# Kernel optimization log

Hardware: AMD Instinct MI355X
Metric: run time of the kernel (lower is better)

## Reference

```python
import jax, jax.numpy as jnp
import numpy as np

B, C, D, H, W = 4, 128, 16, 16, 16
HID = 128
EPS = 1e-5


def setup_inputs() -> dict:
    key = jax.random.key(0)
    ks = jax.random.split(key, 10)
    s = 1.0 / np.sqrt(C)
    return {
        "x": jax.random.normal(ks[0], (B, C, D, H, W), dtype=jnp.float32),
        "Wq": jax.random.normal(ks[1], (HID, C), dtype=jnp.float32) * s,
        "bq": jax.random.normal(ks[2], (HID,), dtype=jnp.float32) * s,
        "Wk": jax.random.normal(ks[3], (HID, C), dtype=jnp.float32) * s,
        "bk": jax.random.normal(ks[4], (HID,), dtype=jnp.float32) * s,
        "Wv": jax.random.normal(ks[5], (HID, C), dtype=jnp.float32) * s,
        "bv": jax.random.normal(ks[6], (HID,), dtype=jnp.float32) * s,
        "bn_weight": jax.random.normal(ks[7], (HID,), dtype=jnp.float32),
        "bn_bias": jax.random.normal(ks[8], (HID,), dtype=jnp.float32),
        "gamma": jax.random.normal(ks[9], (1,), dtype=jnp.float32),
    }


def reference(x, Wq, bq, Wk, bk, Wv, bv, bn_weight, bn_bias, gamma):
    b, c, d, h, w = x.shape
    n = d * h * w
    xf = x.reshape(b, c, n)  # [B, C, N]
    # 1x1 conv3d == per-voxel linear: [B, hid, N]
    q = jnp.einsum("hc,bcn->bnh", Wq, xf) + bq  # [B, N, hid] (query permuted)
    k = jnp.einsum("hc,bcn->bhn", Wk, xf) + bk[None, :, None]  # [B, hid, N]
    v = jnp.einsum("hc,bcn->bhn", Wv, xf) + bv[None, :, None]  # [B, hid, N]
    # unscaled attention scores [B, N, N], softmax over last dim
    attn = jax.nn.softmax(jnp.einsum("bih,bhj->bij", q, k), axis=-1)
    # out[b,h,i] = sum_j v[b,h,j] * attn[b,i,j]
    out = jnp.einsum("bhj,bij->bhi", v, attn)  # [B, hid, N]
    # BatchNorm3d (training mode): per-channel stats over (B, N), biased var
    mean = jnp.mean(out, axis=(0, 2), keepdims=True)
    var = jnp.mean(jnp.square(out - mean), axis=(0, 2), keepdims=True)
    out = (out - mean) * jax.lax.rsqrt(var + EPS)
    out = out * bn_weight[None, :, None] + bn_bias[None, :, None]
    out = gamma[0] * out.reshape(b, c, d, h, w) + x
    return out
```

## Files before the change

kernel.cpp:

```cpp
#include <hip/hip_runtime.h>


#define NV 4096
#define LOG2E 1.44269504088896340736f
#define EPSV 1e-5f

typedef float f32x4 __attribute__((ext_vector_type(4)));
typedef short bf16x8 __attribute__((ext_vector_type(8)));
typedef unsigned short u16x4 __attribute__((ext_vector_type(4)));
typedef unsigned short u16x8 __attribute__((ext_vector_type(8)));
typedef unsigned int u32x2 __attribute__((ext_vector_type(2)));

static __device__ __forceinline__ unsigned short f2bf(float f) {
    union { float f; unsigned u; } v; v.f = f;
    unsigned r = v.u + 0x7FFFu + ((v.u >> 16) & 1u);
    return (unsigned short)(r >> 16);
}
static __device__ __forceinline__ float bf2f(unsigned short u) {
    union { unsigned u; float f; } v; v.u = ((unsigned)u) << 16; return v.f;
}
static __device__ __forceinline__ unsigned fbits(float f) {
    union { float f; unsigned u; } v; v.f = f; return v.u;
}

__global__ __launch_bounds__(256) void projx_kernel(
    const float* __restrict__ x,
    const float* __restrict__ Wq, const float* __restrict__ Wk,
    const float* __restrict__ Wv,
    const float* __restrict__ bq, const float* __restrict__ bk,
    const float* __restrict__ bv,
    unsigned short* __restrict__ Qb, unsigned short* __restrict__ Kb,
    unsigned short* __restrict__ Vb)
{
    __shared__ unsigned short xt[64 * 136];
    __shared__ unsigned short Wl[128 * 136];
    const int bid = blockIdx.x;
    const int m = bid >> 8, b = (bid >> 6) & 3, n0 = (bid & 63) << 6;
    const int t = threadIdx.x, w = t >> 6, lane = t & 63;
    const int quad = lane >> 4, l16 = lane & 15;

    const float* Wm = (m == 0) ? Wq : ((m == 1) ? Wk : Wv);
    const float* bias = (m == 0) ? bq : ((m == 1) ? bk : bv);

    #pragma unroll
    for (int it = 0; it < 8; ++it) {
        const int e = (it << 8) + t;
        const int c = e >> 4, i4 = (e & 15) << 2;
        const float4 xv = *(const float4*)(x + (((b << 7) + c) << 12) + n0 + i4);
        xt[(i4 + 0) * 136 + c] = f2bf(xv.x);
        xt[(i4 + 1) * 136 + c] = f2bf(xv.y);
        xt[(i4 + 2) * 136 + c] = f2bf(xv.z);
        xt[(i4 + 3) * 136 + c] = f2bf(xv.w);
    }
    #pragma unroll
    for (int it = 0; it < 16; ++it) {
        const int idx = it * 1024 + (t << 2);
        const float4 wv4 = *(const float4*)(Wm + idx);
        const int h = idx >> 7, c = idx & 127;
        u16x4 pk;
        pk[0] = f2bf(wv4.x); pk[1] = f2bf(wv4.y);
        pk[2] = f2bf(wv4.z); pk[3] = f2bf(wv4.w);
        *(u16x4*)(Wl + h * 136 + c) = pk;
    }
    __syncthreads();

    bf16x8 af[4];
    {
        const int il = (w << 4) + l16;
        #pragma unroll
        for (int ck = 0; ck < 4; ++ck)
            af[ck] = *(const bf16x8*)(xt + il * 136 + (ck << 5) + (quad << 3));
    }
    if (m == 2) __syncthreads();

    #pragma unroll
    for (int s = 0; s < 8; ++s) {
        const int h = (s << 4) + l16;
        f32x4 acc = {0.f, 0.f, 0.f, 0.f};
        #pragma unroll
        for (int ck = 0; ck < 4; ++ck) {
            const bf16x8 wf = *(const bf16x8*)(Wl + h * 136 + (ck << 5) + (quad << 3));
            acc = __builtin_amdgcn_mfma_f32_16x16x32_bf16(af[ck], wf, acc, 0, 0, 0);
        }
        const float bval = bias[h];
        if (m == 2) {
            #pragma unroll
            for (int r = 0; r < 4; ++r)
                xt[h * 66 + (w << 4) + (quad << 2) + r] = f2bf(acc[r] + bval);
        } else {
            #pragma unroll
            for (int r = 0; r < 4; ++r) {
                float val = acc[r] + bval;
                if (m == 0) val *= LOG2E;
                xt[((w << 4) + (quad << 2) + r) * 136 + h] = f2bf(val);
            }
        }
    }
    __syncthreads();
    if (m == 2) {
        #pragma unroll
        for (int it = 0; it < 32; ++it) {
            const int e = it * 256 + t;
            const int h = e >> 6, il = e & 63;
            Vb[(((b << 7) + h) << 12) + n0 + il] = xt[h * 66 + il];
        }
    } else {
        unsigned short* dst = (m == 0) ? Qb : Kb;
        #pragma unroll
        for (int it = 0; it < 4; ++it) {
            const int e = (it << 8) + t;
            const int row = e >> 4, c8 = (e & 15) << 3;
            *(bf16x8*)(dst + (((b << 12) + n0 + row) << 7) + c8) =
                *(const bf16x8*)(xt + row * 136 + c8);
        }
    }
}

template<int NSL>
__global__ __launch_bounds__(256, 2) void flash_kernel(
    const unsigned short* __restrict__ Qb,
    const unsigned short* __restrict__ Kb,
    const unsigned short* __restrict__ Vb,
    unsigned short* __restrict__ Opart, float* __restrict__ lpart,
    unsigned short* __restrict__ Obuf)
{
    __shared__ unsigned short Kt[64 * 128];
    __shared__ unsigned short Vt[128 * 64];
    __shared__ unsigned short pA[4][32 * 72];
    constexpr int NB = (NSL == 6) ? 768 : NSL * 128;
    const int bid = ((blockIdx.x & 7) * (NB >> 3)) + (blockIdx.x >> 3);
    const int sl = bid >> 7, b = (bid >> 5) & 3, ic = bid & 31;
    const int t = threadIdx.x, w = t >> 6, lane = t & 63;
    const int quad = lane >> 4, l16 = lane & 15;
    const int iw = (ic << 7) + (w << 5);

    int T, joff;
    if constexpr (NSL == 6) {
        T = 11 - (sl >= 4);
        joff = sl * 11 - ((sl >= 5) ? 1 : 0);
    } else {
        T = (NV / NSL) >> 6;
        joff = sl * T;
    }
    const int jbase = joff << 6;
    unsigned short* pAw = pA[w];

    const int ktg = t & 15, ktj = t >> 4;
    const int vtg = t & 7,  vth = t >> 3;
    const int kswz = (ktg ^ ktj) << 3;
    const int vswz = (vtg ^ (vth & 7)) << 3;

    bf16x8 qf[2][4];
    #pragma unroll
    for (int half = 0; half < 2; ++half) {
        const unsigned short* qp =
            Qb + (((b << 12) + iw + (half << 4) + l16) << 7) + (quad << 3);
        #pragma unroll
        for (int ck = 0; ck < 4; ++ck) qf[half][ck] = *(const bf16x8*)(qp + (ck << 5));
    }
    f32x4 Oacc[2][8];
    #pragma unroll
    for (int half = 0; half < 2; ++half)
        #pragma unroll
        for (int s = 0; s < 8; ++s) Oacc[half][s] = (f32x4){0.f, 0.f, 0.f, 0.f};
    float lsum0 = 0.f, lsum1 = 0.f;

    const unsigned short* Kbb = Kb + ((long)b << 19);
    const unsigned short* Vbb = Vb + ((long)b << 19);
    const int T8 = T;

    bf16x8 sk[4], sv[4];
    #pragma unroll
    for (int r = 0; r < 4; ++r)
        sk[r] = *(const bf16x8*)(Kbb + ((jbase + (r << 4) + ktj) << 7) + (ktg << 3));
    #pragma unroll
    for (int r = 0; r < 4; ++r)
        sv[r] = *(const bf16x8*)(Vbb + (((r << 5) + vth) << 12) + jbase + (vtg << 3));

    for (int t8 = 0; t8 < T8; ++t8) {
        const int j0 = jbase + (t8 << 6);

        __syncthreads();
        #pragma unroll
        for (int r = 0; r < 4; ++r)
            *(bf16x8*)(Kt + (((r << 4) + ktj) << 7) + kswz) = sk[r];
        #pragma unroll
        for (int r = 0; r < 4; ++r)
            *(bf16x8*)(Vt + (((r << 5) + vth) << 6) + vswz) = sv[r];
        __syncthreads();

        if (t8 + 1 < T8) {
            const int j1 = j0 + 64;
            #pragma unroll
            for (int r = 0; r < 4; ++r)
                sk[r] = *(const bf16x8*)(Kbb + ((j1 + (r << 4) + ktj) << 7) + (ktg << 3));
            #pragma unroll
            for (int r = 0; r < 4; ++r)
                sv[r] = *(const bf16x8*)(Vbb + (((r << 5) + vth) << 12) + j1 + (vtg << 3));
        }

        #pragma unroll
        for (int js = 0; js < 4; ++js) {
            bf16x8 kf[4];
            const int krow = ((js << 4) + l16) << 7;
            #pragma unroll
            for (int ck = 0; ck < 4; ++ck)
                kf[ck] = *(const bf16x8*)(Kt + krow + ((((ck << 2) + quad) ^ l16) << 3));
            f32x4 a0 = {0.f, 0.f, 0.f, 0.f}, a1 = {0.f, 0.f, 0.f, 0.f};
            #pragma unroll
            for (int ck = 0; ck < 4; ++ck) {
                a0 = __builtin_amdgcn_mfma_f32_16x16x32_bf16(kf[ck], qf[0][ck], a0, 0, 0, 0);
                a1 = __builtin_amdgcn_mfma_f32_16x16x32_bf16(kf[ck], qf[1][ck], a1, 0, 0, 0);
            }
            f32x4 e0, e1;
            #pragma unroll
            for (int r = 0; r < 4; ++r) {
                e0[r] = __builtin_amdgcn_exp2f(a0[r]);
                e1[r] = __builtin_amdgcn_exp2f(a1[r]);
            }
            lsum0 += (e0[0] + e0[1]) + (e0[2] + e0[3]);
            lsum1 += (e1[0] + e1[1]) + (e1[2] + e1[3]);
            u32x2 pk0, pk1;
            pk0[0] = __builtin_amdgcn_perm(fbits(e0[1]), fbits(e0[0]), 0x07060302u);
            pk0[1] = __builtin_amdgcn_perm(fbits(e0[3]), fbits(e0[2]), 0x07060302u);
            pk1[0] = __builtin_amdgcn_perm(fbits(e1[1]), fbits(e1[0]), 0x07060302u);
            pk1[1] = __builtin_amdgcn_perm(fbits(e1[3]), fbits(e1[2]), 0x07060302u);
            const int jc = (js << 4) + (quad << 2);
            *(u32x2*)(pAw + l16 * 72 + jc)        = pk0;
            *(u32x2*)(pAw + (16 + l16) * 72 + jc) = pk1;
        }
        bf16x8 pf[2][2];
        #pragma unroll
        for (int half = 0; half < 2; ++half)
            #pragma unroll
            for (int kh = 0; kh < 2; ++kh)
                pf[half][kh] = *(const bf16x8*)(pAw + ((half << 4) + l16) * 72 +
                                                (kh << 5) + (quad << 3));
        #pragma unroll
        for (int s = 0; s < 8; ++s) {
            const int vrow = ((s << 4) + l16) << 6;
            const bf16x8 v0 = *(const bf16x8*)(Vt + vrow + ((quad ^ (l16 & 7)) << 3));
            const bf16x8 v1 = *(const bf16x8*)(Vt + vrow + (((4 + quad) ^ (l16 & 7)) << 3));
            Oacc[0][s] = __builtin_amdgcn_mfma_f32_16x16x32_bf16(v0, pf[0][0], Oacc[0][s], 0, 0, 0);
            Oacc[0][s] = __builtin_amdgcn_mfma_f32_16x16x32_bf16(v1, pf[0][1], Oacc[0][s], 0, 0, 0);
            Oacc[1][s] = __builtin_amdgcn_mfma_f32_16x16x32_bf16(v0, pf[1][0], Oacc[1][s], 0, 0, 0);
            Oacc[1][s] = __builtin_amdgcn_mfma_f32_16x16x32_bf16(v1, pf[1][1], Oacc[1][s], 0, 0, 0);
        }
    }

    float l0 = lsum0; l0 += __shfl_xor(l0, 16); l0 += __shfl_xor(l0, 32);
    float l1 = lsum1; l1 += __shfl_xor(l1, 16); l1 += __shfl_xor(l1, 32);

    if (NSL == 1) {
        const float rl0 = 1.f / l0, rl1 = 1.f / l1;
        #pragma unroll
        for (int s = 0; s < 8; ++s)
            #pragma unroll
            for (int r = 0; r < 4; ++r) {
                const int h = (s << 4) + (quad << 2) + r;
                Obuf[(((b << 7) + h) << 12) + iw + l16]      = f2bf(Oacc[0][s][r] * rl0);
                Obuf[(((b << 7) + h) << 12) + iw + 16 + l16] = f2bf(Oacc[1][s][r] * rl1);
            }
    } else {
        const int slb = (sl << 2) + b;
        if (quad == 0) {
            lpart[(slb << 12) + iw + l16]      = l0;
            lpart[(slb << 12) + iw + 16 + l16] = l1;
        }
        unsigned short* Ob = Opart + ((long)slb << 19);
        #pragma unroll
        for (int half = 0; half < 2; ++half)
            #pragma unroll
            for (int s = 0; s < 8; ++s)
                #pragma unroll
                for (int r = 0; r < 4; ++r) {
                    const int h = (s << 4) + (quad << 2) + r;
                    Ob[(h << 12) + iw + (half << 4) + l16] = f2bf(Oacc[half][s][r]);
                }
    }
}

template<int NSL>
__global__ __launch_bounds__(1024) void mf_kernel(
    const unsigned short* __restrict__ Opart, const float* __restrict__ lpart,
    const float* __restrict__ x, const float* __restrict__ bnw,
    const float* __restrict__ bnb, const float* __restrict__ gammap,
    float* __restrict__ out)
{
    const int h = blockIdx.x;
    const int t = threadIdx.x;
    const int b = t >> 8;
    const int i0 = (t & 255) << 4;

    float A[16], L[16];
    #pragma unroll
    for (int k = 0; k < 16; ++k) { A[k] = 0.f; L[k] = 0.f; }
    #pragma unroll
    for (int sl = 0; sl < NSL; ++sl) {
        const int slb = (sl << 2) + b;
        const u16x8 u0 = *(const u16x8*)(Opart + ((long)slb << 19) + ((long)h << 12) + i0);
        const u16x8 u1 = *(const u16x8*)(Opart + ((long)slb << 19) + ((long)h << 12) + i0 + 8);
        const float* lp = lpart + (slb << 12) + i0;
        #pragma unroll
        for (int k = 0; k < 8; ++k) { A[k] += bf2f(u0[k]); A[8 + k] += bf2f(u1[k]); }
        #pragma unroll
        for (int k = 0; k < 4; ++k) {
            const float4 lv = *(const float4*)(lp + (k << 2));
            L[(k << 2) + 0] += lv.x; L[(k << 2) + 1] += lv.y;
            L[(k << 2) + 2] += lv.z; L[(k << 2) + 3] += lv.w;
        }
    }
    float o[16], s = 0.f, ss = 0.f;
    #pragma unroll
    for (int k = 0; k < 16; ++k) {
        o[k] = A[k] / L[k];
        s += o[k]; ss += o[k] * o[k];
    }
    #pragma unroll
    for (int off = 32; off; off >>= 1) {
        s  += __shfl_down(s, off);
        ss += __shfl_down(ss, off);
    }
    __shared__ float rs[16], rss[16], fin[2];
    const int wid = t >> 6;
    if ((t & 63) == 0) { rs[wid] = s; rss[wid] = ss; }
    __syncthreads();
    if (t == 0) {
        float s2 = 0.f, ss2 = 0.f;
        #pragma unroll
        for (int k = 0; k < 16; ++k) { s2 += rs[k]; ss2 += rss[k]; }
        fin[0] = s2; fin[1] = ss2;
    }
    __syncthreads();
    const float inv = 1.f / 16384.f;
    const float mean = fin[0] * inv;
    const float var  = fin[1] * inv - mean * mean;
    const float g = gammap[0];
    const float scale = bnw[h] * rsqrtf(var + EPSV);
    const float a  = g * scale;
    const float bb = g * (bnb[h] - mean * scale);

    const float* xp = x + (((b << 7) + h) << 12) + i0;
    float* op = out + (((b << 7) + h) << 12) + i0;
    #pragma unroll
    for (int k = 0; k < 4; ++k) {
        const float4 xv = *(const float4*)(xp + (k << 2));
        float4 r;
        r.x = o[(k << 2) + 0] * a + bb + xv.x;
        r.y = o[(k << 2) + 1] * a + bb + xv.y;
        r.z = o[(k << 2) + 2] * a + bb + xv.z;
        r.w = o[(k << 2) + 3] * a + bb + xv.w;
        *(float4*)(op + (k << 2)) = r;
    }
}

__global__ __launch_bounds__(1024) void mf1_kernel(
    const unsigned short* __restrict__ Obuf,
    const float* __restrict__ x, const float* __restrict__ bnw,
    const float* __restrict__ bnb, const float* __restrict__ gammap,
    float* __restrict__ out)
{
    const int h = blockIdx.x;
    const int t = threadIdx.x;
    const int b = t >> 8;
    const int i0 = (t & 255) << 4;
    const u16x8 u0 = *(const u16x8*)(Obuf + (((b << 7) + h) << 12) + i0);
    const u16x8 u1 = *(const u16x8*)(Obuf + (((b << 7) + h) << 12) + i0 + 8);
    float o[16], s = 0.f, ss = 0.f;
    #pragma unroll
    for (int k = 0; k < 8; ++k) { o[k] = bf2f(u0[k]); o[8 + k] = bf2f(u1[k]); }
    #pragma unroll
    for (int k = 0; k < 16; ++k) { s += o[k]; ss += o[k] * o[k]; }
    #pragma unroll
    for (int off = 32; off; off >>= 1) {
        s  += __shfl_down(s, off);
        ss += __shfl_down(ss, off);
    }
    __shared__ float rs[16], rss[16], fin[2];
    const int wid = t >> 6;
    if ((t & 63) == 0) { rs[wid] = s; rss[wid] = ss; }
    __syncthreads();
    if (t == 0) {
        float s2 = 0.f, ss2 = 0.f;
        #pragma unroll
        for (int k = 0; k < 16; ++k) { s2 += rs[k]; ss2 += rss[k]; }
        fin[0] = s2; fin[1] = ss2;
    }
    __syncthreads();
    const float inv = 1.f / 16384.f;
    const float mean = fin[0] * inv;
    const float var  = fin[1] * inv - mean * mean;
    const float g = gammap[0];
    const float scale = bnw[h] * rsqrtf(var + EPSV);
    const float a  = g * scale;
    const float bb = g * (bnb[h] - mean * scale);
    const float* xp = x + (((b << 7) + h) << 12) + i0;
    float* op = out + (((b << 7) + h) << 12) + i0;
    #pragma unroll
    for (int k = 0; k < 4; ++k) {
        const float4 xv = *(const float4*)(xp + (k << 2));
        float4 r;
        r.x = o[(k << 2) + 0] * a + bb + xv.x;
        r.y = o[(k << 2) + 1] * a + bb + xv.y;
        r.z = o[(k << 2) + 2] * a + bb + xv.z;
        r.w = o[(k << 2) + 3] * a + bb + xv.w;
        *(float4*)(op + (k << 2)) = r;
    }
}

extern "C" void kernel_launch(void* const* d_in, const int* in_sizes, int n_in,
                              void* d_out, int out_size, void* d_ws, size_t ws_size,
                              hipStream_t stream) {
    const float* x   = (const float*)d_in[0];
    const float* Wq  = (const float*)d_in[1];
    const float* bq  = (const float*)d_in[2];
    const float* Wk  = (const float*)d_in[3];
    const float* bk  = (const float*)d_in[4];
    const float* Wv  = (const float*)d_in[5];
    const float* bv  = (const float*)d_in[6];
    const float* bnw = (const float*)d_in[7];
    const float* bnb = (const float*)d_in[8];
    const float* gam = (const float*)d_in[9];
    float* out = (float*)d_out;

    char* ws = (char*)d_ws;
    unsigned short* Obuf = (unsigned short*)(ws);
    unsigned short* Qb   = (unsigned short*)(ws + (4u  << 20));
    unsigned short* Kb   = (unsigned short*)(ws + (8u  << 20));
    unsigned short* Vb   = (unsigned short*)(ws + (12u << 20));
    float*          lpart = (float*)(ws + (16u << 20) + (128u << 10));
    unsigned short* Opart = (unsigned short*)(ws + (17u << 20));

    int nsl = 1;
    if      (ws_size >= (17ull << 20) + (32ull << 20)) nsl = 6;
    else if (ws_size >= (17ull << 20) + (16ull << 20)) nsl = 4;
    else if (ws_size >= (17ull << 20) + (8ull  << 20)) nsl = 2;

    projx_kernel<<<768, 256, 0, stream>>>(x, Wq, Wk, Wv, bq, bk, bv, Qb, Kb, Vb);
    if (nsl == 6) {
        flash_kernel<6><<<768, 256, 0, stream>>>(Qb, Kb, Vb, Opart, lpart, Obuf);
        mf_kernel<6><<<128, 1024, 0, stream>>>(Opart, lpart, x, bnw, bnb, gam, out);
    } else if (nsl == 4) {
        flash_kernel<4><<<512, 256, 0, stream>>>(Qb, Kb, Vb, Opart, lpart, Obuf);
        mf_kernel<4><<<128, 1024, 0, stream>>>(Opart, lpart, x, bnw, bnb, gam, out);
    } else if (nsl == 2) {
        flash_kernel<2><<<256, 256, 0, stream>>>(Qb, Kb, Vb, Opart, lpart, Obuf);
        mf_kernel<2><<<128, 1024, 0, stream>>>(Opart, lpart, x, bnw, bnb, gam, out);
    } else {
        flash_kernel<1><<<128, 256, 0, stream>>>(Qb, Kb, Vb, Opart, lpart, Obuf);
        mf1_kernel<<<128, 1024, 0, stream>>>(Obuf, x, bnw, bnb, gam, out);
    }
}
```

Measured before the change: 148.7 us.

## Use 32x32x16 MFMA with permlane32 swap to keep P in registers

Rewrites the flash attention inner loop around 32x32x16 bf16 MFMA tiles. The exponentiated scores are repacked in registers with v_permlane32_swap, so P is fed to the PV matmul without the per-wave LDS staging buffer. It also adds s_setprio around the MFMA sections and drops the 6-way split, so the default path becomes the 4-way split with 512 blocks. This cuts LDS traffic and instruction count per tile, at the cost of higher register pressure from 64 accumulator floats plus the 16-wide score tile, and a different load balance without the 6-split.

```diff
diff --git a/kernel.cpp b/kernel.cpp
--- a/kernel.cpp
+++ b/kernel.cpp
@@ -6,10 +6,10 @@
 #define EPSV 1e-5f
 
 typedef float f32x4 __attribute__((ext_vector_type(4)));
+typedef float f32x16 __attribute__((ext_vector_type(16)));
 typedef short bf16x8 __attribute__((ext_vector_type(8)));
 typedef unsigned short u16x4 __attribute__((ext_vector_type(4)));
 typedef unsigned short u16x8 __attribute__((ext_vector_type(8)));
-typedef unsigned int u32x2 __attribute__((ext_vector_type(2)));
 
 static __device__ __forceinline__ unsigned short f2bf(float f) {
     union { float f; unsigned u; } v; v.f = f;
@@ -126,48 +126,36 @@
 {
     __shared__ unsigned short Kt[64 * 128];
     __shared__ unsigned short Vt[128 * 64];
-    __shared__ unsigned short pA[4][32 * 72];
-    constexpr int NB = (NSL == 6) ? 768 : NSL * 128;
+    constexpr int NB = NSL * 128;
     const int bid = ((blockIdx.x & 7) * (NB >> 3)) + (blockIdx.x >> 3);
     const int sl = bid >> 7, b = (bid >> 5) & 3, ic = bid & 31;
     const int t = threadIdx.x, w = t >> 6, lane = t & 63;
-    const int quad = lane >> 4, l16 = lane & 15;
+    const int l32 = lane & 31, hi = lane >> 5;
     const int iw = (ic << 7) + (w << 5);
 
-    int T, joff;
-    if constexpr (NSL == 6) {
-        T = 11 - (sl >= 4);
-        joff = sl * 11 - ((sl >= 5) ? 1 : 0);
-    } else {
-        T = (NV / NSL) >> 6;
-        joff = sl * T;
-    }
-    const int jbase = joff << 6;
-    unsigned short* pAw = pA[w];
+    const int T = (NV / NSL) >> 6;
+    const int jbase = sl * T << 6;
 
     const int ktg = t & 15, ktj = t >> 4;
     const int vtg = t & 7,  vth = t >> 3;
     const int kswz = (ktg ^ ktj) << 3;
     const int vswz = (vtg ^ (vth & 7)) << 3;
 
-    bf16x8 qf[2][4];
-    #pragma unroll
-    for (int half = 0; half < 2; ++half) {
-        const unsigned short* qp =
-            Qb + (((b << 12) + iw + (half << 4) + l16) << 7) + (quad << 3);
-        #pragma unroll
-        for (int ck = 0; ck < 4; ++ck) qf[half][ck] = *(const bf16x8*)(qp + (ck << 5));
-    }
-    f32x4 Oacc[2][8];
-    #pragma unroll
-    for (int half = 0; half < 2; ++half)
-        #pragma unroll
-        for (int s = 0; s < 8; ++s) Oacc[half][s] = (f32x4){0.f, 0.f, 0.f, 0.f};
-    float lsum0 = 0.f, lsum1 = 0.f;
+    bf16x8 qf[8];
+    {
+        const unsigned short* qp = Qb + (((b << 12) + iw + l32) << 7) + (hi << 3);
+        #pragma unroll
+        for (int kc = 0; kc < 8; ++kc) qf[kc] = *(const bf16x8*)(qp + (kc << 4));
+    }
+    f32x16 Oacc[4];
+    #pragma unroll
+    for (int ht = 0; ht < 4; ++ht)
+        #pragma unroll
+        for (int r = 0; r < 16; ++r) Oacc[ht][r] = 0.f;
+    float lsum = 0.f;
 
     const unsigned short* Kbb = Kb + ((long)b << 19);
     const unsigned short* Vbb = Vb + ((long)b << 19);
-    const int T8 = T;
 
     bf16x8 sk[4], sv[4];
     #pragma unroll
@@ -177,7 +165,7 @@
     for (int r = 0; r < 4; ++r)
         sv[r] = *(const bf16x8*)(Vbb + (((r << 5) + vth) << 12) + jbase + (vtg << 3));
 
-    for (int t8 = 0; t8 < T8; ++t8) {
+    for (int t8 = 0; t8 < T; ++t8) {
         const int j0 = jbase + (t8 << 6);
 
         __syncthreads();
@@ -189,7 +177,7 @@
             *(bf16x8*)(Vt + (((r << 5) + vth) << 6) + vswz) = sv[r];
         __syncthreads();
 
-        if (t8 + 1 < T8) {
+        if (t8 + 1 < T) {
             const int j1 = j0 + 64;
             #pragma unroll
             for (int r = 0; r < 4; ++r)
@@ -200,83 +188,77 @@
         }
 
         #pragma unroll
-        for (int js = 0; js < 4; ++js) {
-            bf16x8 kf[4];
-            const int krow = ((js << 4) + l16) << 7;
-            #pragma unroll
-            for (int ck = 0; ck < 4; ++ck)
-                kf[ck] = *(const bf16x8*)(Kt + krow + ((((ck << 2) + quad) ^ l16) << 3));
-            f32x4 a0 = {0.f, 0.f, 0.f, 0.f}, a1 = {0.f, 0.f, 0.f, 0.f};
-            #pragma unroll
-            for (int ck = 0; ck < 4; ++ck) {
-                a0 = __builtin_amdgcn_mfma_f32_16x16x32_bf16(kf[ck], qf[0][ck], a0, 0, 0, 0);
-                a1 = __builtin_amdgcn_mfma_f32_16x16x32_bf16(kf[ck], qf[1][ck], a1, 0, 0, 0);
+        for (int jt = 0; jt < 2; ++jt) {
+            const unsigned short* kr = Kt + (((jt << 5) + l32) << 7);
+            f32x16 a;
+            #pragma unroll
+            for (int r = 0; r < 16; ++r) a[r] = 0.f;
+            __builtin_amdgcn_s_setprio(1);
+            #pragma unroll
+            for (int kc = 0; kc < 8; ++kc) {
+                const bf16x8 kf = *(const bf16x8*)(kr + ((((kc << 1) + hi) ^ (l32 & 15)) << 3));
+                a = __builtin_amdgcn_mfma_f32_32x32x16_bf16(kf, qf[kc], a, 0, 0, 0);
             }
-            f32x4 e0, e1;
-            #pragma unroll
-            for (int r = 0; r < 4; ++r) {
-                e0[r] = __builtin_amdgcn_exp2f(a0[r]);
-                e1[r] = __builtin_amdgcn_exp2f(a1[r]);
+            __builtin_amdgcn_s_setprio(0);
+            float e[16];
+            #pragma unroll
+            for (int r = 0; r < 16; ++r) e[r] = __builtin_amdgcn_exp2f(a[r]);
+            lsum += ((e[0] + e[1]) + (e[2] + e[3])) + ((e[4] + e[5]) + (e[6] + e[7]))
+                  + ((e[8] + e[9]) + (e[10] + e[11])) + ((e[12] + e[13]) + (e[14] + e[15]));
+            unsigned wd[8];
+            #pragma unroll
+            for (int g = 0; g < 8; ++g)
+                wd[g] = __builtin_amdgcn_perm(fbits(e[2 * g + 1]), fbits(e[2 * g]),
+                                              0x07060302u);
+            unsigned a0 = wd[0], a2 = wd[2];
+            asm("v_permlane32_swap_b32 %0, %1" : "+v"(a0), "+v"(a2));
+            unsigned a1 = wd[1], a3 = wd[3];
+            asm("v_permlane32_swap_b32 %0, %1" : "+v"(a1), "+v"(a3));
+            unsigned b0 = wd[4], b2 = wd[6];
+            asm("v_permlane32_swap_b32 %0, %1" : "+v"(b0), "+v"(b2));
+            unsigned b1 = wd[5], b3 = wd[7];
+            asm("v_permlane32_swap_b32 %0, %1" : "+v"(b1), "+v"(b3));
+            union PW { unsigned w[4]; bf16x8 v; };
+            PW p0, p1;
+            p0.w[0] = a0; p0.w[1] = a1; p0.w[2] = a2; p0.w[3] = a3;
+            p1.w[0] = b0; p1.w[1] = b1; p1.w[2] = b2; p1.w[3] = b3;
+            const bf16x8 pa0 = p0.v, pa1 = p1.v;
+            __builtin_amdgcn_s_setprio(1);
+            #pragma unroll
+            for (int ht = 0; ht < 4; ++ht) {
+                const unsigned short* vr = Vt + (((ht << 5) + l32) << 6);
+                const bf16x8 v0 = *(const bf16x8*)(vr + ((((jt << 2) + hi) ^ (l32 & 7)) << 3));
+                const bf16x8 v1 = *(const bf16x8*)(vr + ((((jt << 2) + 2 + hi) ^ (l32 & 7)) << 3));
+                Oacc[ht] = __builtin_amdgcn_mfma_f32_32x32x16_bf16(v0, pa0, Oacc[ht], 0, 0, 0);
+                Oacc[ht] = __builtin_amdgcn_mfma_f32_32x32x16_bf16(v1, pa1, Oacc[ht], 0, 0, 0);
             }
-            lsum0 += (e0[0] + e0[1]) + (e0[2] + e0[3]);
-            lsum1 += (e1[0] + e1[1]) + (e1[2] + e1[3]);
-            u32x2 pk0, pk1;
-            pk0[0] = __builtin_amdgcn_perm(fbits(e0[1]), fbits(e0[0]), 0x07060302u);
-            pk0[1] = __builtin_amdgcn_perm(fbits(e0[3]), fbits(e0[2]), 0x07060302u);
-            pk1[0] = __builtin_amdgcn_perm(fbits(e1[1]), fbits(e1[0]), 0x07060302u);
-            pk1[1] = __builtin_amdgcn_perm(fbits(e1[3]), fbits(e1[2]), 0x07060302u);
-            const int jc = (js << 4) + (quad << 2);
-            *(u32x2*)(pAw + l16 * 72 + jc)        = pk0;
-            *(u32x2*)(pAw + (16 + l16) * 72 + jc) = pk1;
-        }
-        bf16x8 pf[2][2];
-        #pragma unroll
-        for (int half = 0; half < 2; ++half)
-            #pragma unroll
-            for (int kh = 0; kh < 2; ++kh)
-                pf[half][kh] = *(const bf16x8*)(pAw + ((half << 4) + l16) * 72 +
-                                                (kh << 5) + (quad << 3));
-        #pragma unroll
-        for (int s = 0; s < 8; ++s) {
-            const int vrow = ((s << 4) + l16) << 6;
-            const bf16x8 v0 = *(const bf16x8*)(Vt + vrow + ((quad ^ (l16 & 7)) << 3));
-            const bf16x8 v1 = *(const bf16x8*)(Vt + vrow + (((4 + quad) ^ (l16 & 7)) << 3));
-            Oacc[0][s] = __builtin_amdgcn_mfma_f32_16x16x32_bf16(v0, pf[0][0], Oacc[0][s], 0, 0, 0);
-            Oacc[0][s] = __builtin_amdgcn_mfma_f32_16x16x32_bf16(v1, pf[0][1], Oacc[0][s], 0, 0, 0);
-            Oacc[1][s] = __builtin_amdgcn_mfma_f32_16x16x32_bf16(v0, pf[1][0], Oacc[1][s], 0, 0, 0);
-            Oacc[1][s] = __builtin_amdgcn_mfma_f32_16x16x32_bf16(v1, pf[1][1], Oacc[1][s], 0, 0, 0);
-        }
-    }
-
-    float l0 = lsum0; l0 += __shfl_xor(l0, 16); l0 += __shfl_xor(l0, 32);
-    float l1 = lsum1; l1 += __shfl_xor(l1, 16); l1 += __shfl_xor(l1, 32);
+            __builtin_amdgcn_s_setprio(0);
+        }
+    }
+
+    float l = lsum;
+    l += __shfl_xor(l, 32);
 
     if (NSL == 1) {
-        const float rl0 = 1.f / l0, rl1 = 1.f / l1;
-        #pragma unroll
-        for (int s = 0; s < 8; ++s)
-            #pragma unroll
-            for (int r = 0; r < 4; ++r) {
-                const int h = (s << 4) + (quad << 2) + r;
-                Obuf[(((b << 7) + h) << 12) + iw + l16]      = f2bf(Oacc[0][s][r] * rl0);
-                Obuf[(((b << 7) + h) << 12) + iw + 16 + l16] = f2bf(Oacc[1][s][r] * rl1);
+        const float rl = 1.f / l;
+        #pragma unroll
+        for (int ht = 0; ht < 4; ++ht)
+            #pragma unroll
+            for (int r = 0; r < 16; ++r) {
+                const int h = (ht << 5) + (hi << 2) + (r & 3) + ((r >> 2) << 3);
+                Obuf[(((b << 7) + h) << 12) + iw + l32] = f2bf(Oacc[ht][r] * rl);
             }
     } else {
         const int slb = (sl << 2) + b;
-        if (quad == 0) {
-            lpart[(slb << 12) + iw + l16]      = l0;
-            lpart[(slb << 12) + iw + 16 + l16] = l1;
-        }
+        if (!hi) lpart[(slb << 12) + iw + l32] = l;
         unsigned short* Ob = Opart + ((long)slb << 19);
         #pragma unroll
-        for (int half = 0; half < 2; ++half)
-            #pragma unroll
-            for (int s = 0; s < 8; ++s)
-                #pragma unroll
-                for (int r = 0; r < 4; ++r) {
-                    const int h = (s << 4) + (quad << 2) + r;
-                    Ob[(h << 12) + iw + (half << 4) + l16] = f2bf(Oacc[half][s][r]);
-                }
+        for (int ht = 0; ht < 4; ++ht)
+            #pragma unroll
+            for (int r = 0; r < 16; ++r) {
+                const int h = (ht << 5) + (hi << 2) + (r & 3) + ((r >> 2) << 3);
+                Ob[(h << 12) + iw + l32] = f2bf(Oacc[ht][r]);
+            }
     }
 }
 
@@ -432,15 +414,11 @@
     unsigned short* Opart = (unsigned short*)(ws + (17u << 20));
 
     int nsl = 1;
-    if      (ws_size >= (17ull << 20) + (32ull << 20)) nsl = 6;
-    else if (ws_size >= (17ull << 20) + (16ull << 20)) nsl = 4;
+    if      (ws_size >= (17ull << 20) + (16ull << 20)) nsl = 4;
     else if (ws_size >= (17ull << 20) + (8ull  << 20)) nsl = 2;
 
     projx_kernel<<<768, 256, 0, stream>>>(x, Wq, Wk, Wv, bq, bk, bv, Qb, Kb, Vb);
-    if (nsl == 6) {
-        flash_kernel<6><<<768, 256, 0, stream>>>(Qb, Kb, Vb, Opart, lpart, Obuf);
-        mf_kernel<6><<<128, 1024, 0, stream>>>(Opart, lpart, x, bnw, bnb, gam, out);
-    } else if (nsl == 4) {
+    if (nsl == 4) {
         flash_kernel<4><<<512, 256, 0, stream>>>(Qb, Kb, Vb, Opart, lpart, Obuf);
         mf_kernel<4><<<128, 1024, 0, stream>>>(Opart, lpart, x, bnw, bnb, gam, out);
     } else if (nsl == 2) {
```

After: 140.0 us. 5.8% less time.
